# Optimization experiments

Hardware: AMD Instinct MI355X
Metric: run time of the kernel (lower is better)

## Reference

```python
import jax, jax.numpy as jnp
import numpy as np

N = 20000      # bs * n_node
E = 400000     # n_edge
D = 128        # input_nf = hidden_nf
C = 4          # n_channel
ED = 16        # edges_in_d
HS = 4         # mlp_hidden_scale
COORD_MAX = 10.0


def setup_inputs() -> dict:
    key = jax.random.key(0)
    ks = jax.random.split(key, 10)
    h = jax.random.normal(ks[0], (N, D), dtype=jnp.float32)
    coord = jax.random.normal(ks[1], (N, C, 3), dtype=jnp.float32)
    edge_index = jax.random.randint(ks[2], (2, E), 0, N)
    edge_attr = jax.random.normal(ks[3], (E, ED), dtype=jnp.float32)
    kv_in = D + C * C + ED
    Wq = jax.random.normal(ks[4], (D, D), dtype=jnp.float32) * float(1.0 / np.sqrt(D))
    bq = jnp.zeros((D,), dtype=jnp.float32)
    Wkv = jax.random.normal(ks[5], (kv_in, 2 * D), dtype=jnp.float32) * float(1.0 / np.sqrt(kv_in))
    bkv = jnp.zeros((2 * D,), dtype=jnp.float32)
    Wc1 = jax.random.normal(ks[6], (D, HS * D), dtype=jnp.float32) * float(1.0 / np.sqrt(D))
    Wc2 = jax.random.normal(ks[7], (HS * D, C), dtype=jnp.float32) * 0.001  # xavier gain=0.001
    return {"h": h, "coord": coord, "edge_index": edge_index, "edge_attr": edge_attr,
            "Wq": Wq, "bq": bq, "Wkv": Wkv, "bkv": bkv, "Wc1": Wc1, "Wc2": Wc2}


def reference(h, coord, edge_index, edge_attr, Wq, bq, Wkv, bkv, Wc1, Wc2):
    row, col = edge_index[0], edge_index[1]
    n_nodes = h.shape[0]

    # coord2radial (norm_type=None)
    coord_diff = coord[row] - coord[col]                     # [E, C, 3]
    radial = jnp.einsum('ecd,efd->ecf', coord_diff, coord_diff)  # [E, C, C]
    radial = radial.reshape(radial.shape[0], -1)             # [E, C*C]

    # att_model: gather, QKV, scatter-softmax over destination node `row`
    q = h[row] @ Wq + bq                                      # [E, D]
    target_feat = jnp.concatenate([radial, h[col], edge_attr], axis=1)
    kv = target_feat @ Wkv + bkv                               # [E, 2D]
    k, v = kv[:, 0::2], kv[:, 1::2]                            # [E, D] each
    alpha = jnp.sum(q * k, axis=1)                             # [E]
    m = jax.ops.segment_max(alpha, row, num_segments=n_nodes)
    e = jnp.exp(alpha - m[row])
    s = jax.ops.segment_sum(e, row, num_segments=n_nodes)
    att = e / s[row]                                           # [E]

    # node_model (dropout in eval mode = identity)
    agg = jax.ops.segment_sum(att[:, None] * v, row, num_segments=n_nodes)
    h_out = h + agg

    # coord_model: coord_mlp is Linear(no bias) -> SiLU -> Linear(no bias)
    coord_v = att[:, None] * (jax.nn.silu(v @ Wc1) @ Wc2)      # [E, C]
    trans = coord_diff * coord_v[:, :, None]                   # [E, C, 3]
    cagg = jax.ops.segment_sum(trans, row, num_segments=n_nodes)
    coord_out = coord + jnp.clip(cagg, -COORD_MAX, COORD_MAX)

    return (h_out, coord_out, att)
```

## Files before the change

### kernel.cpp

```cpp
#include <hip/hip_runtime.h>

typedef unsigned short u16;
typedef __attribute__((ext_vector_type(8))) short short8;
typedef __attribute__((ext_vector_type(4))) float floatx4;

constexpr int N_ = 20000;
constexpr int E_ = 400000;

#define DEV __device__ __forceinline__

DEV float bf2f(u16 u) { union { unsigned int i; float f; } x; x.i = ((unsigned int)u) << 16; return x.f; }
DEV u16 f2bf(float f) {
    union { unsigned int i; float f; } x; x.f = f;
    unsigned int i = x.i;
    unsigned int r = i + 0x7FFFu + ((i >> 16) & 1u);
    return (u16)(r >> 16);
}
DEV unsigned int fenc(float f) {
    unsigned int i = __float_as_uint(f);
    return (i & 0x80000000u) ? ~i : (i | 0x80000000u);
}
DEV float fdec(unsigned int u) {
    return (u & 0x80000000u) ? __uint_as_float(u ^ 0x80000000u) : __uint_as_float(~u);
}

__global__ __launch_bounds__(256) void k_zero(unsigned int* p, int n) {
    int i = blockIdx.x * 256 + threadIdx.x;
    if (i < n) p[i] = 0u;
}

__global__ __launch_bounds__(256) void k_prep0(
    const float* __restrict__ Wq, const float* __restrict__ bq, const float* __restrict__ Wkv,
    float* __restrict__ M_r, float* __restrict__ M_ea, float* __restrict__ br, float* __restrict__ bea) {
    int o = blockIdx.x * 256 + threadIdx.x;
    if (o < 2048) {
        int k = o >> 4, j = o & 15;
        float acc = 0.f;
        for (int d = 0; d < 128; ++d) acc += Wq[k * 128 + d] * Wkv[(size_t)j * 256 + 2 * d];
        M_r[k * 16 + j] = acc;
    } else if (o < 4096) {
        int k = (o - 2048) >> 4, j = o & 15;
        float acc = 0.f;
        for (int d = 0; d < 128; ++d) acc += Wq[k * 128 + d] * Wkv[(size_t)(144 + j) * 256 + 2 * d];
        M_ea[k * 16 + j] = acc;
    } else if (o < 4112) {
        int j = o - 4096;
        float acc = 0.f;
        for (int d = 0; d < 128; ++d) acc += bq[d] * Wkv[(size_t)j * 256 + 2 * d];
        br[j] = acc;
    } else if (o < 4128) {
        int j = o - 4112;
        float acc = 0.f;
        for (int d = 0; d < 128; ++d) acc += bq[d] * Wkv[(size_t)(144 + j) * 256 + 2 * d];
        bea[j] = acc;
    }
}

__global__ __launch_bounds__(256) void k_prepA(
    const float* __restrict__ Wq, const float* __restrict__ Wkv,
    const float* __restrict__ M_r, const float* __restrict__ M_ea,
    u16* __restrict__ WAf_hi, u16* __restrict__ WAf_lo) {
    int idx = blockIdx.x * 256 + threadIdx.x;
    if (idx >= 6656) return;
    int lane = idx & 63;
    int tkc = idx >> 6;
    int t = tkc >> 2, kc = tkc & 3;
    int col = t * 16 + (lane & 15);
    int k0 = kc * 32 + (lane >> 4) * 8;
#pragma unroll
    for (int j = 0; j < 8; ++j) {
        int k = k0 + j;
        float v;
        if (col < 128)      v = Wq[(size_t)k * 128 + col];
        else if (col < 256) v = Wkv[(size_t)(16 + k) * 256 + 2 * (col - 128)];
        else if (col < 384) v = Wkv[(size_t)(16 + k) * 256 + 2 * (col - 256) + 1];
        else if (col < 400) v = M_r[k * 16 + (col - 384)];
        else                v = M_ea[k * 16 + (col - 400)];
        u16 hi = f2bf(v);
        WAf_hi[(size_t)idx * 8 + j] = hi;
        WAf_lo[(size_t)idx * 8 + j] = f2bf(v - bf2f(hi));
    }
}

__global__ __launch_bounds__(256) void k_prepB(
    const float* __restrict__ Wc1, u16* __restrict__ Wc1f_hi, u16* __restrict__ Wc1f_lo) {
    int idx = blockIdx.x * 256 + threadIdx.x;
    int lane = idx & 63;
    int tkc = idx >> 6;
    int t = tkc >> 2, kc = tkc & 3;
    int jc = t * 16 + (lane & 15);
    int k0 = kc * 32 + (lane >> 4) * 8;
#pragma unroll
    for (int j = 0; j < 8; ++j) {
        float v = Wc1[(size_t)(k0 + j) * 512 + jc];
        u16 hi = f2bf(v);
        Wc1f_hi[(size_t)idx * 8 + j] = hi;
        Wc1f_lo[(size_t)idx * 8 + j] = f2bf(v - bf2f(hi));
    }
}

__global__ __launch_bounds__(256) void k_gemmA(
    const float* __restrict__ h, const u16* __restrict__ WAf_hi, const u16* __restrict__ WAf_lo,
    const float* __restrict__ bq, const float* __restrict__ bkv,
    const float* __restrict__ br, const float* __restrict__ bea,
    float* __restrict__ hq, float* __restrict__ k_h, u16* __restrict__ v_hi16, u16* __restrict__ v_lo16,
    float* __restrict__ hqWkr, float* __restrict__ hqWkea) {
    __shared__ __align__(16) u16 hhi[16][128];
    __shared__ __align__(16) u16 hlo[16][128];
    int t = threadIdx.x;
    int n0 = blockIdx.x * 16;
    for (int i = t; i < 2048; i += 256) {
        int n = i >> 7, d = i & 127;
        float x = h[(size_t)(n0 + n) * 128 + d];
        u16 hi = f2bf(x);
        hhi[n][d] = hi;
        hlo[n][d] = f2bf(x - bf2f(hi));
    }
    __syncthreads();
    int wv = t >> 6, lane = t & 63;
    int m = lane & 15, q = lane >> 4;
    short8 ahi[4], alo[4];
#pragma unroll
    for (int kc = 0; kc < 4; ++kc) {
        ahi[kc] = *(const short8*)(&hhi[m][kc * 32 + q * 8]);
        alo[kc] = *(const short8*)(&hlo[m][kc * 32 + q * 8]);
    }
    for (int tt = wv; tt < 26; tt += 4) {
        floatx4 acc = {0.f, 0.f, 0.f, 0.f};
#pragma unroll
        for (int kc = 0; kc < 4; ++kc) {
            size_t fo = ((size_t)(tt * 4 + kc) * 64 + lane) * 8;
            short8 bhi = *(const short8*)(WAf_hi + fo);
            short8 blo = *(const short8*)(WAf_lo + fo);
            acc = __builtin_amdgcn_mfma_f32_16x16x32_bf16(ahi[kc], bhi, acc, 0, 0, 0);
            acc = __builtin_amdgcn_mfma_f32_16x16x32_bf16(ahi[kc], blo, acc, 0, 0, 0);
            acc = __builtin_amdgcn_mfma_f32_16x16x32_bf16(alo[kc], bhi, acc, 0, 0, 0);
        }
        int col = tt * 16 + m;
        if (tt < 8) {
            float b = bq[col];
#pragma unroll
            for (int reg = 0; reg < 4; ++reg)
                hq[(size_t)(n0 + q * 4 + reg) * 128 + col] = acc[reg] + b;
        } else if (tt < 16) {
            int d = col - 128;
            float b = bkv[2 * d];
#pragma unroll
            for (int reg = 0; reg < 4; ++reg)
                k_h[(size_t)(n0 + q * 4 + reg) * 128 + d] = acc[reg] + b;
        } else if (tt < 24) {
            int d = col - 256;
            float b = bkv[2 * d + 1];
#pragma unroll
            for (int reg = 0; reg < 4; ++reg) {
                float vf = acc[reg] + b;
                u16 hi = f2bf(vf);
                size_t o = (size_t)(n0 + q * 4 + reg) * 128 + d;
                v_hi16[o] = hi;
                v_lo16[o] = f2bf(vf - bf2f(hi));
            }
        } else if (tt == 24) {
            float b = br[m];
#pragma unroll
            for (int reg = 0; reg < 4; ++reg)
                hqWkr[(size_t)(n0 + q * 4 + reg) * 16 + m] = acc[reg] + b;
        } else {
            float b = bea[m];
#pragma unroll
            for (int reg = 0; reg < 4; ++reg)
                hqWkea[(size_t)(n0 + q * 4 + reg) * 16 + m] = acc[reg] + b;
        }
    }
}

__global__ __launch_bounds__(256) void k_gemmB(
    const u16* __restrict__ v_hi16, const u16* __restrict__ v_lo16,
    const u16* __restrict__ Wc1f_hi, const u16* __restrict__ Wc1f_lo,
    u16* __restrict__ vWc1h) {
    int t = threadIdx.x;
    int n0 = blockIdx.x * 16;
    int wv = t >> 6, lane = t & 63;
    int m = lane & 15, q = lane >> 4;
    short8 ahi[4], alo[4];
#pragma unroll
    for (int kc = 0; kc < 4; ++kc) {
        size_t o = (size_t)(n0 + m) * 128 + kc * 32 + q * 8;
        ahi[kc] = *(const short8*)(v_hi16 + o);
        alo[kc] = *(const short8*)(v_lo16 + o);
    }
    for (int tt = wv; tt < 32; tt += 4) {
        floatx4 acc = {0.f, 0.f, 0.f, 0.f};
#pragma unroll
        for (int kc = 0; kc < 4; ++kc) {
            size_t fo = ((size_t)(tt * 4 + kc) * 64 + lane) * 8;
            short8 bhi = *(const short8*)(Wc1f_hi + fo);
            short8 blo = *(const short8*)(Wc1f_lo + fo);
            acc = __builtin_amdgcn_mfma_f32_16x16x32_bf16(ahi[kc], bhi, acc, 0, 0, 0);
            acc = __builtin_amdgcn_mfma_f32_16x16x32_bf16(ahi[kc], blo, acc, 0, 0, 0);
            acc = __builtin_amdgcn_mfma_f32_16x16x32_bf16(alo[kc], bhi, acc, 0, 0, 0);
        }
        int jc = tt * 16 + m;
#pragma unroll
        for (int reg = 0; reg < 4; ++reg)
            vWc1h[(size_t)(n0 + q * 4 + reg) * 512 + jc] = f2bf(acc[reg]);
    }
}

__global__ __launch_bounds__(256) void k_composites(
    const float* __restrict__ Wkv, const float* __restrict__ Wc1,
    float* __restrict__ Cr, float* __restrict__ Cea) {
    int o = blockIdx.x * 256 + threadIdx.x;
    int half = o >> 13;
    int j = (o >> 9) & 15;
    int jc = o & 511;
    int row = half ? (144 + j) : j;
    float acc = 0.f;
    for (int d = 0; d < 128; ++d)
        acc += Wkv[(size_t)row * 256 + 2 * d + 1] * Wc1[(size_t)d * 512 + jc];
    (half ? Cea : Cr)[j * 512 + jc] = acc;
}

__global__ __launch_bounds__(256) void k_hist_both(const int* __restrict__ edge_index,
                                                   int* __restrict__ countsR, int* __restrict__ countsC) {
    int i = blockIdx.x * 256 + threadIdx.x;
    if (i < E_) {
        atomicAdd(&countsR[edge_index[i]], 1);
        atomicAdd(&countsC[edge_index[E_ + i]], 1);
    }
}

__global__ __launch_bounds__(1024) void k_scan2(
    const int* __restrict__ countsR, const int* __restrict__ countsC,
    int* __restrict__ offR, int* __restrict__ curR,
    int* __restrict__ offC, int* __restrict__ curC) {
    __shared__ int wtotR[16], wtotC[16];
    int t = threadIdx.x;
    int lane = t & 63, wv = t >> 6;
    int baseR = 0, baseC = 0;
    for (int start = 0; start < N_; start += 1024) {
        int i = start + t;
        int oR = (i < N_) ? countsR[i] : 0;
        int oC = (i < N_) ? countsC[i] : 0;
        int vR = oR, vC = oC;
#pragma unroll
        for (int off = 1; off < 64; off <<= 1) {
            int xR = __shfl_up(vR, off);
            int xC = __shfl_up(vC, off);
            if (lane >= off) { vR += xR; vC += xC; }
        }
        if (lane == 63) { wtotR[wv] = vR; wtotC[wv] = vC; }
        __syncthreads();
        int wbR = 0, totR = 0, wbC = 0, totC = 0;
#pragma unroll
        for (int k = 0; k < 16; ++k) {
            int wR = wtotR[k], wC = wtotC[k];
            if (k < wv) { wbR += wR; wbC += wC; }
            totR += wR; totC += wC;
        }
        if (i < N_) {
            int eR = baseR + wbR + vR - oR;
            int eC = baseC + wbC + vC - oC;
            offR[i] = eR; curR[i] = eR;
            offC[i] = eC; curC[i] = eC;
        }
        baseR += totR; baseC += totC;
        __syncthreads();
    }
    if (t == 0) { offR[N_] = baseR; offC[N_] = baseC; }
}

__global__ void k_fill_both(const int* __restrict__ edge_index,
                            int* __restrict__ curR, int* __restrict__ curC,
                            int* __restrict__ edge_ids, int* __restrict__ edge_ids2,
                            int* __restrict__ rank2) {
    int i = blockIdx.x * 256 + threadIdx.x;
    if (i < E_) {
        int r = edge_index[i], c = edge_index[E_ + i];
        int pr = atomicAdd(&curR[r], 1);
        edge_ids[pr] = i;
        int pc = atomicAdd(&curC[c], 1);
        edge_ids2[pc] = i;
        rank2[i] = pc;
    }
}

__global__ __launch_bounds__(256) void k_alpha_csr(
    const int* __restrict__ edge_index, const int* __restrict__ edge_ids,
    const float* __restrict__ coord, const float* __restrict__ edge_attr,
    const float* __restrict__ hq, const float* __restrict__ k_h,
    const float* __restrict__ hqWkr, const float* __restrict__ hqWkea,
    float* __restrict__ alpha_pos) {
    int wv = threadIdx.x >> 6, lane = threadIdx.x & 63;
    int p = blockIdx.x * 4 + wv;
    int e = edge_ids[p];
    int row = edge_index[e], col = edge_index[E_ + e];
    float s = hq[(size_t)row * 128 + lane] * k_h[(size_t)col * 128 + lane] +
              hq[(size_t)row * 128 + 64 + lane] * k_h[(size_t)col * 128 + 64 + lane];
    if (lane < 16) {
        int c = lane >> 2, f = lane & 3;
        float rj = 0.f;
#pragma unroll
        for (int x = 0; x < 3; ++x) {
            float a = coord[(size_t)row * 12 + c * 3 + x] - coord[(size_t)col * 12 + c * 3 + x];
            float b = coord[(size_t)row * 12 + f * 3 + x] - coord[(size_t)col * 12 + f * 3 + x];
            rj += a * b;
        }
        s += hqWkr[(size_t)row * 16 + lane] * rj;
    } else if (lane < 32) {
        int j = lane - 16;
        s += hqWkea[(size_t)row * 16 + j] * edge_attr[(size_t)e * 16 + j];
    }
#pragma unroll
    for (int mm = 32; mm; mm >>= 1) s += __shfl_xor(s, mm);
    if (lane == 0) alpha_pos[p] = s;
}

__global__ __launch_bounds__(256, 3) void k_edge_z(
    const int* __restrict__ edge_index, const int* __restrict__ edge_ids2,
    const float* __restrict__ coord, const float* __restrict__ edge_attr,
    const float* __restrict__ Cr, const float* __restrict__ Cea, const float* __restrict__ Wc2,
    const u16* __restrict__ vWc1h, float* __restrict__ Z) {
    __shared__ __align__(16) u16 Bf[32 * 64 * 8];
    __shared__ __align__(16) float W2[512 * 4];
    __shared__ __align__(16) u16 Xs[64][16];
    int t = threadIdx.x;
    for (int i = t; i < 2048; i += 256) {
        int tile = i >> 6, ln = i & 63;
        int jc = tile * 16 + (ln & 15);
        int k0 = (ln >> 4) * 8;
#pragma unroll
        for (int j = 0; j < 8; ++j) {
            int k = k0 + j;
            float v = (k < 16) ? Cr[(size_t)k * 512 + jc] : Cea[(size_t)(k - 16) * 512 + jc];
            Bf[i * 8 + j] = f2bf(v);
        }
    }
    for (int i = t; i < 2048; i += 256) W2[i] = Wc2[i];
    __syncthreads();
    int wv = t >> 6, lane = t & 63;
    int m = lane & 15, q = lane >> 4;
    int wid = blockIdx.x * 4 + wv;
    int nw = gridDim.x * 4;
    for (int ti = wid; ti < E_ / 16; ti += nw) {
        int p0 = ti * 16;
#pragma unroll
        for (int i4 = 0; i4 < 4; ++i4) {
            int e = edge_ids2[p0 + i4 * 4 + q];
            int row = edge_index[e], col = edge_index[E_ + e];
            float d = 0.f;
            if (m < 12) d = coord[(size_t)row * 12 + m] - coord[(size_t)col * 12 + m];
            int base = lane & 48;
            int c3 = (m >> 2) * 3, f3 = (m & 3) * 3;
            float r = 0.f;
#pragma unroll
            for (int x = 0; x < 3; ++x) r += __shfl(d, base + c3 + x) * __shfl(d, base + f3 + x);
            Xs[wv * 16 + i4 * 4 + q][m] = f2bf(r);
        }
        short8 afrag;
        if (q < 2) {
            afrag = *(const short8*)(&Xs[wv * 16 + m][q * 8]);
        } else {
            int em = edge_ids2[p0 + m];
            const float* ea = edge_attr + (size_t)em * 16 + (q - 2) * 8;
#pragma unroll
            for (int j = 0; j < 8; ++j) afrag[j] = (short)f2bf(ea[j]);
        }
        int cr[4];
#pragma unroll
        for (int reg = 0; reg < 4; ++reg) cr[reg] = edge_index[E_ + edge_ids2[p0 + q * 4 + reg]];
        float cvp[4][4];
#pragma unroll
        for (int reg = 0; reg < 4; ++reg)
#pragma unroll
            for (int c = 0; c < 4; ++c) cvp[reg][c] = 0.f;
        for (int tt = 0; tt < 32; ++tt) {
            short8 bfrag = *(const short8*)(Bf + (size_t)(tt * 64 + lane) * 8);
            floatx4 acc = {0.f, 0.f, 0.f, 0.f};
            acc = __builtin_amdgcn_mfma_f32_16x16x32_bf16(afrag, bfrag, acc, 0, 0, 0);
            int jc = tt * 16 + m;
            float4 w2 = *(const float4*)(W2 + jc * 4);
#pragma unroll
            for (int reg = 0; reg < 4; ++reg) {
                float u = acc[reg] + bf2f(vWc1h[(size_t)cr[reg] * 512 + jc]);
                float su = u / (1.f + __expf(-u));
                cvp[reg][0] += su * w2.x;
                cvp[reg][1] += su * w2.y;
                cvp[reg][2] += su * w2.z;
                cvp[reg][3] += su * w2.w;
            }
        }
#pragma unroll
        for (int mm = 1; mm < 16; mm <<= 1)
#pragma unroll
            for (int reg = 0; reg < 4; ++reg)
#pragma unroll
                for (int c = 0; c < 4; ++c) cvp[reg][c] += __shfl_xor(cvp[reg][c], mm);
        if (m < 4) {
#pragma unroll
            for (int reg = 0; reg < 4; ++reg)
                Z[(size_t)(p0 + q * 4 + reg) * 4 + m] = cvp[reg][m];
        }
    }
}

__global__ __launch_bounds__(256) void k_node_main(
    const int* __restrict__ edge_index, const int* __restrict__ offsets, const int* __restrict__ edge_ids,
    const int* __restrict__ rank2, const float* __restrict__ alpha_pos,
    const u16* __restrict__ v_h16, const float* __restrict__ Z,
    const float* __restrict__ coord, const float* __restrict__ edge_attr, const float* __restrict__ h,
    const float* __restrict__ Wkv, float* __restrict__ h_out, float* __restrict__ coord_out,
    float* __restrict__ att_out) {
    __shared__ float attL[4][128];
    int wv = threadIdx.x >> 6, lane = threadIdx.x & 63;
    int n = blockIdx.x * 4 + wv;
    int beg = offsets[n], end = offsets[n + 1];
    float cn[12];
#pragma unroll
    for (int i = 0; i < 12; ++i) cn[i] = coord[(size_t)n * 12 + i];
    float mloc = -3.402823466e38f;
    for (int i = beg + lane; i < end; i += 64) mloc = fmaxf(mloc, alpha_pos[i]);
#pragma unroll
    for (int mm = 32; mm; mm >>= 1) mloc = fmaxf(mloc, __shfl_xor(mloc, mm));
    float sloc = 0.f;
    for (int i = beg + lane; i < end; i += 64) sloc += __expf(alpha_pos[i] - mloc);
#pragma unroll
    for (int mm = 32; mm; mm >>= 1) sloc += __shfl_xor(sloc, mm);
    float inv_s = (end > beg) ? 1.f / sloc : 0.f;
    float raggr[16], eaggr[16], cagg[12];
#pragma unroll
    for (int j = 0; j < 16; ++j) { raggr[j] = 0.f; eaggr[j] = 0.f; }
#pragma unroll
    for (int j = 0; j < 12; ++j) cagg[j] = 0.f;
    for (int ii = lane; ii < end - beg; ii += 64) {
        int i = beg + ii;
        int e = edge_ids[i];
        int col = edge_index[E_ + e];
        float att = __expf(alpha_pos[i] - mloc) * inv_s;
        if (ii < 128) attL[wv][ii] = att;
        att_out[e] = att;
        float cd[12];
#pragma unroll
        for (int x = 0; x < 12; ++x) cd[x] = cn[x] - coord[(size_t)col * 12 + x];
#pragma unroll
        for (int c = 0; c < 4; ++c)
#pragma unroll
            for (int f = 0; f < 4; ++f) {
                float r = cd[c * 3] * cd[f * 3] + cd[c * 3 + 1] * cd[f * 3 + 1] + cd[c * 3 + 2] * cd[f * 3 + 2];
                raggr[c * 4 + f] += att * r;
            }
#pragma unroll
        for (int j = 0; j < 16; ++j) eaggr[j] += att * edge_attr[(size_t)e * 16 + j];
        size_t zb = (size_t)rank2[e] * 4;
        float cv0 = att * Z[zb + 0];
        float cv1 = att * Z[zb + 1];
        float cv2 = att * Z[zb + 2];
        float cv3 = att * Z[zb + 3];
#pragma unroll
        for (int x = 0; x < 3; ++x) {
            cagg[0 + x] += cv0 * cd[0 + x];
            cagg[3 + x] += cv1 * cd[3 + x];
            cagg[6 + x] += cv2 * cd[6 + x];
            cagg[9 + x] += cv3 * cd[9 + x];
        }
    }
#pragma unroll
    for (int mm = 32; mm; mm >>= 1) {
#pragma unroll
        for (int j = 0; j < 16; ++j) {
            raggr[j] += __shfl_xor(raggr[j], mm);
            eaggr[j] += __shfl_xor(eaggr[j], mm);
        }
#pragma unroll
        for (int j = 0; j < 12; ++j) cagg[j] += __shfl_xor(cagg[j], mm);
    }
    float agg0 = 0.f, agg1 = 0.f;
    int deg = end - beg;
    for (int i = 0; i < deg; ++i) {
        int e = edge_ids[beg + i];
        int col = edge_index[E_ + e];
        float att = (i < 128) ? attL[wv][i] : __expf(alpha_pos[beg + i] - mloc) * inv_s;
        agg0 += att * bf2f(v_h16[(size_t)col * 128 + lane]);
        agg1 += att * bf2f(v_h16[(size_t)col * 128 + 64 + lane]);
    }
#pragma unroll
    for (int g = 0; g < 2; ++g) {
        int dd = g * 64 + lane;
        float acc = g ? agg1 : agg0;
#pragma unroll
        for (int j = 0; j < 16; ++j) {
            acc += raggr[j] * Wkv[(size_t)j * 256 + 2 * dd + 1];
            acc += eaggr[j] * Wkv[(size_t)(144 + j) * 256 + 2 * dd + 1];
        }
        h_out[(size_t)n * 128 + dd] = h[(size_t)n * 128 + dd] + acc;
    }
    if (lane == 0) {
#pragma unroll
        for (int i = 0; i < 12; ++i) {
            float v = fminf(fmaxf(cagg[i], -10.f), 10.f);
            coord_out[(size_t)n * 12 + i] = cn[i] + v;
        }
    }
}

__global__ __launch_bounds__(256) void k_hq_slow(
    const float* __restrict__ h, const float* __restrict__ Wq, const float* __restrict__ bq,
    float* __restrict__ hq) {
    int idx = blockIdx.x * 256 + threadIdx.x;
    int n = idx >> 7, d = idx & 127;
    float acc = 0.f;
    for (int k = 0; k < 128; ++k) acc += h[(size_t)n * 128 + k] * Wq[k * 128 + d];
    hq[idx] = acc + bq[d];
}

__global__ __launch_bounds__(256) void k_alpha_slow(
    const int* __restrict__ edge_index, const float* __restrict__ coord,
    const float* __restrict__ edge_attr, const float* __restrict__ h,
    const float* __restrict__ Wkv, const float* __restrict__ bkv,
    const float* __restrict__ hq, float* __restrict__ alpha, unsigned int* __restrict__ m) {
    __shared__ float tf[4][160];
    int wv = threadIdx.x >> 6, lane = threadIdx.x & 63;
    int e = blockIdx.x * 4 + wv;
    int row = edge_index[e], col = edge_index[E_ + e];
    if (lane < 16) {
        int c = lane >> 2, f = lane & 3;
        float rj = 0.f;
#pragma unroll
        for (int x = 0; x < 3; ++x) {
            float a = coord[(size_t)row * 12 + c * 3 + x] - coord[(size_t)col * 12 + c * 3 + x];
            float b = coord[(size_t)row * 12 + f * 3 + x] - coord[(size_t)col * 12 + f * 3 + x];
            rj += a * b;
        }
        tf[wv][lane] = rj;
    }
    for (int f = lane; f < 128; f += 64) tf[wv][16 + f] = h[(size_t)col * 128 + f];
    if (lane >= 48) tf[wv][144 + lane - 48] = edge_attr[(size_t)e * 16 + lane - 48];
    __syncthreads();
    float k0 = bkv[2 * lane], k1 = bkv[2 * (64 + lane)];
    for (int f = 0; f < 160; ++f) {
        float tfv = tf[wv][f];
        k0 += tfv * Wkv[f * 256 + 2 * lane];
        k1 += tfv * Wkv[f * 256 + 128 + 2 * lane];
    }
    float p = hq[(size_t)row * 128 + lane] * k0 + hq[(size_t)row * 128 + 64 + lane] * k1;
#pragma unroll
    for (int mm = 32; mm; mm >>= 1) p += __shfl_xor(p, mm);
    if (lane == 0) {
        alpha[e] = p;
        atomicMax(&m[row], fenc(p));
    }
}

__global__ __launch_bounds__(256) void k_expsum_slow(
    const int* __restrict__ edge_index, const float* __restrict__ alpha,
    const unsigned int* __restrict__ m, float* __restrict__ s) {
    int e = blockIdx.x * 256 + threadIdx.x;
    if (e < E_) {
        int row = edge_index[e];
        atomicAdd(&s[row], __expf(alpha[e] - fdec(m[row])));
    }
}

__global__ __launch_bounds__(256) void k_edge2_slow(
    const int* __restrict__ edge_index, const float* __restrict__ coord,
    const float* __restrict__ edge_attr, const float* __restrict__ h,
    const float* __restrict__ Wkv, const float* __restrict__ bkv,
    const float* __restrict__ Wc1, const float* __restrict__ Wc2,
    const float* __restrict__ alpha, const unsigned int* __restrict__ m, const float* __restrict__ s,
    float* __restrict__ agg, float* __restrict__ cagg, float* __restrict__ att_out) {
    __shared__ float tf[4][160];
    __shared__ float vsh[4][128];
    int wv = threadIdx.x >> 6, lane = threadIdx.x & 63;
    int e = blockIdx.x * 4 + wv;
    int row = edge_index[e], col = edge_index[E_ + e];
    if (lane < 16) {
        int c = lane >> 2, f = lane & 3;
        float rj = 0.f;
#pragma unroll
        for (int x = 0; x < 3; ++x) {
            float a = coord[(size_t)row * 12 + c * 3 + x] - coord[(size_t)col * 12 + c * 3 + x];
            float b = coord[(size_t)row * 12 + f * 3 + x] - coord[(size_t)col * 12 + f * 3 + x];
            rj += a * b;
        }
        tf[wv][lane] = rj;
    }
    for (int f = lane; f < 128; f += 64) tf[wv][16 + f] = h[(size_t)col * 128 + f];
    if (lane >= 48) tf[wv][144 + lane - 48] = edge_attr[(size_t)e * 16 + lane - 48];
    __syncthreads();
    float v0 = bkv[2 * lane + 1], v1 = bkv[2 * (64 + lane) + 1];
    for (int f = 0; f < 160; ++f) {
        float tfv = tf[wv][f];
        v0 += tfv * Wkv[f * 256 + 2 * lane + 1];
        v1 += tfv * Wkv[f * 256 + 129 + 2 * lane];
    }
    float att = __expf(alpha[e] - fdec(m[row])) / s[row];
    atomicAdd(&agg[(size_t)row * 128 + lane], att * v0);
    atomicAdd(&agg[(size_t)row * 128 + 64 + lane], att * v1);
    vsh[wv][lane] = v0;
    vsh[wv][64 + lane] = v1;
    __syncthreads();
    float cv[4] = {0.f, 0.f, 0.f, 0.f};
    for (int g = 0; g < 8; ++g) {
        int jc = g * 64 + lane;
        float u = 0.f;
        for (int dd = 0; dd < 128; ++dd) u += vsh[wv][dd] * Wc1[dd * 512 + jc];
        float su = u / (1.f + __expf(-u));
#pragma unroll
        for (int c = 0; c < 4; ++c) cv[c] += su * Wc2[jc * 4 + c];
    }
#pragma unroll
    for (int mm = 32; mm; mm >>= 1)
#pragma unroll
        for (int c = 0; c < 4; ++c) cv[c] += __shfl_xor(cv[c], mm);
    if (lane < 12) {
        int c = lane / 3;
        float cd = coord[(size_t)row * 12 + lane] - coord[(size_t)col * 12 + lane];
        atomicAdd(&cagg[(size_t)row * 12 + lane], att * cv[c] * cd);
    }
    if (lane == 0) att_out[e] = att;
}

__global__ __launch_bounds__(256) void k_final_slow(
    const float* __restrict__ h, const float* __restrict__ coord,
    const float* __restrict__ agg, const float* __restrict__ cagg,
    float* __restrict__ h_out, float* __restrict__ coord_out) {
    int idx = blockIdx.x * 256 + threadIdx.x;
    h_out[idx] = h[idx] + agg[idx];
    if (idx < N_ * 12) {
        float v = fminf(fmaxf(cagg[idx], -10.f), 10.f);
        coord_out[idx] = coord[idx] + v;
    }
}

extern "C" void kernel_launch(void* const* d_in, const int* in_sizes, int n_in,
                              void* d_out, int out_size, void* d_ws, size_t ws_size,
                              hipStream_t stream) {
    (void)in_sizes; (void)n_in; (void)out_size;
    const float* h          = (const float*)d_in[0];
    const float* coord      = (const float*)d_in[1];
    const int*   edge_index = (const int*)d_in[2];
    const float* edge_attr  = (const float*)d_in[3];
    const float* Wq         = (const float*)d_in[4];
    const float* bq         = (const float*)d_in[5];
    const float* Wkv        = (const float*)d_in[6];
    const float* bkv        = (const float*)d_in[7];
    const float* Wc1        = (const float*)d_in[8];
    const float* Wc2        = (const float*)d_in[9];

    float* out = (float*)d_out;
    float* h_out = out;
    float* coord_out = out + (size_t)N_ * 128;
    float* att_out = coord_out + (size_t)N_ * 12;

    char* w = (char*)d_ws;
    size_t off = 0;
    auto alloc = [&](size_t bytes) -> void* {
        void* p = w + off;
        off += (bytes + 255) & ~(size_t)255;
        return p;
    };
    int* countsR   = (int*)alloc((size_t)2 * N_ * 4);
    int* countsC   = countsR + N_;
    float* hq      = (float*)alloc((size_t)N_ * 128 * 4);
    float* k_h     = (float*)alloc((size_t)N_ * 128 * 4);
    u16*   v_h16   = (u16*)alloc((size_t)N_ * 128 * 2);
    u16*   v_lo16  = (u16*)alloc((size_t)N_ * 128 * 2);
    u16*   vWc1h   = (u16*)alloc((size_t)N_ * 512 * 2);
    float* hqWkr   = (float*)alloc((size_t)N_ * 16 * 4);
    float* hqWkea  = (float*)alloc((size_t)N_ * 16 * 4);
    float* alphaP  = (float*)alloc((size_t)E_ * 4);
    float* Z       = (float*)alloc((size_t)E_ * 4 * 4);
    float* Cr      = (float*)alloc(16 * 512 * 4);
    float* Cea     = (float*)alloc(16 * 512 * 4);
    float* M_r     = (float*)alloc(128 * 16 * 4);
    float* M_ea    = (float*)alloc(128 * 16 * 4);
    float* br      = (float*)alloc(16 * 4);
    float* bea     = (float*)alloc(16 * 4);
    u16* WAf_hi    = (u16*)alloc((size_t)26 * 4 * 64 * 8 * 2);
    u16* WAf_lo    = (u16*)alloc((size_t)26 * 4 * 64 * 8 * 2);
    u16* Wc1f_hi   = (u16*)alloc((size_t)32 * 4 * 64 * 8 * 2);
    u16* Wc1f_lo   = (u16*)alloc((size_t)32 * 4 * 64 * 8 * 2);
    int* offsetsR  = (int*)alloc((size_t)(N_ + 1) * 4);
    int* cursorR   = (int*)alloc((size_t)N_ * 4);
    int* edge_ids  = (int*)alloc((size_t)E_ * 4);
    int* offsetsC  = (int*)alloc((size_t)(N_ + 1) * 4);
    int* cursorC   = (int*)alloc((size_t)N_ * 4);
    int* edge_ids2 = (int*)alloc((size_t)E_ * 4);
    int* rank2     = (int*)alloc((size_t)E_ * 4);
    size_t fast_req = off;

    if (ws_size >= fast_req) {
        hipLaunchKernelGGL(k_zero, dim3((2 * N_ + 255) / 256), dim3(256), 0, stream,
                           (unsigned int*)countsR, 2 * N_);
        hipLaunchKernelGGL(k_hist_both, dim3((E_ + 255) / 256), dim3(256), 0, stream,
                           edge_index, countsR, countsC);
        hipLaunchKernelGGL(k_scan2, dim3(1), dim3(1024), 0, stream,
                           countsR, countsC, offsetsR, cursorR, offsetsC, cursorC);
        hipLaunchKernelGGL(k_fill_both, dim3((E_ + 255) / 256), dim3(256), 0, stream,
                           edge_index, cursorR, cursorC, edge_ids, edge_ids2, rank2);
        hipLaunchKernelGGL(k_prep0, dim3(17), dim3(256), 0, stream,
                           Wq, bq, Wkv, M_r, M_ea, br, bea);
        hipLaunchKernelGGL(k_prepA, dim3(26), dim3(256), 0, stream,
                           Wq, Wkv, M_r, M_ea, WAf_hi, WAf_lo);
        hipLaunchKernelGGL(k_prepB, dim3(32), dim3(256), 0, stream,
                           Wc1, Wc1f_hi, Wc1f_lo);
        hipLaunchKernelGGL(k_composites, dim3(64), dim3(256), 0, stream, Wkv, Wc1, Cr, Cea);
        hipLaunchKernelGGL(k_gemmA, dim3(N_ / 16), dim3(256), 0, stream,
                           h, WAf_hi, WAf_lo, bq, bkv, br, bea,
                           hq, k_h, v_h16, v_lo16, hqWkr, hqWkea);
        hipLaunchKernelGGL(k_gemmB, dim3(N_ / 16), dim3(256), 0, stream,
                           v_h16, v_lo16, Wc1f_hi, Wc1f_lo, vWc1h);
        hipLaunchKernelGGL(k_alpha_csr, dim3(E_ / 4), dim3(256), 0, stream,
                           edge_index, edge_ids, coord, edge_attr, hq, k_h, hqWkr, hqWkea, alphaP);
        hipLaunchKernelGGL(k_edge_z, dim3(768), dim3(256), 0, stream,
                           edge_index, edge_ids2, coord, edge_attr, Cr, Cea, Wc2, vWc1h, Z);
        hipLaunchKernelGGL(k_node_main, dim3(N_ / 4), dim3(256), 0, stream,
                           edge_index, offsetsR, edge_ids, rank2, alphaP, v_h16, Z,
                           coord, edge_attr, h, Wkv, h_out, coord_out, att_out);
    } else {
        off = 0;
        float* s        = (float*)alloc((size_t)N_ * 4);
        unsigned int* m = (unsigned int*)alloc((size_t)N_ * 4);
        float* agg      = (float*)alloc((size_t)N_ * 128 * 4);
        float* cagg     = (float*)alloc((size_t)N_ * 12 * 4);
        size_t zb       = off;
        float* hq2      = (float*)alloc((size_t)N_ * 128 * 4);
        float* alpha2   = (float*)alloc((size_t)E_ * 4);
        int zero_n = (int)(zb / 4);
        hipLaunchKernelGGL(k_zero, dim3((zero_n + 255) / 256), dim3(256), 0, stream,
                           (unsigned int*)s, zero_n);
        hipLaunchKernelGGL(k_hq_slow, dim3(N_ * 128 / 256), dim3(256), 0, stream, h, Wq, bq, hq2);
        hipLaunchKernelGGL(k_alpha_slow, dim3(E_ / 4), dim3(256), 0, stream,
                           edge_index, coord, edge_attr, h, Wkv, bkv, hq2, alpha2, m);
        hipLaunchKernelGGL(k_expsum_slow, dim3((E_ + 255) / 256), dim3(256), 0, stream,
                           edge_index, alpha2, m, s);
        hipLaunchKernelGGL(k_edge2_slow, dim3(E_ / 4), dim3(256), 0, stream,
                           edge_index, coord, edge_attr, h, Wkv, bkv, Wc1, Wc2,
                           alpha2, m, s, agg, cagg, att_out);
        hipLaunchKernelGGL(k_final_slow, dim3(N_ * 128 / 256), dim3(256), 0, stream,
                           h, coord, agg, cagg, h_out, coord_out);
    }
}
```

Measured before the change: 810.6 us.

## Swizzle vWc1 layout for vector loads and index Z by edge id

```diff
diff --git a/kernel.cpp b/kernel.cpp
--- a/kernel.cpp
+++ b/kernel.cpp
@@ -176,7 +176,7 @@
 __global__ __launch_bounds__(256) void k_gemmB(
     const u16* __restrict__ v_hi16, const u16* __restrict__ v_lo16,
     const u16* __restrict__ Wc1f_hi, const u16* __restrict__ Wc1f_lo,
-    u16* __restrict__ vWc1h) {
+    u16* __restrict__ vWc1s) {
     int t = threadIdx.x;
     int n0 = blockIdx.x * 16;
     int wv = t >> 6, lane = t & 63;
@@ -199,10 +199,9 @@
             acc = __builtin_amdgcn_mfma_f32_16x16x32_bf16(ahi[kc], blo, acc, 0, 0, 0);
             acc = __builtin_amdgcn_mfma_f32_16x16x32_bf16(alo[kc], bhi, acc, 0, 0, 0);
         }
-        int jc = tt * 16 + m;
 #pragma unroll
         for (int reg = 0; reg < 4; ++reg)
-            vWc1h[(size_t)(n0 + q * 4 + reg) * 512 + jc] = f2bf(acc[reg]);
+            vWc1s[(size_t)(n0 + q * 4 + reg) * 512 + m * 32 + tt] = f2bf(acc[reg]);
     }
 }
 
@@ -271,8 +270,7 @@
 
 __global__ void k_fill_both(const int* __restrict__ edge_index,
                             int* __restrict__ curR, int* __restrict__ curC,
-                            int* __restrict__ edge_ids, int* __restrict__ edge_ids2,
-                            int* __restrict__ rank2) {
+                            int* __restrict__ edge_ids, int* __restrict__ edge_ids2) {
     int i = blockIdx.x * 256 + threadIdx.x;
     if (i < E_) {
         int r = edge_index[i], c = edge_index[E_ + i];
@@ -280,7 +278,6 @@
         edge_ids[pr] = i;
         int pc = atomicAdd(&curC[c], 1);
         edge_ids2[pc] = i;
-        rank2[i] = pc;
     }
 }
 
@@ -319,7 +316,7 @@
     const int* __restrict__ edge_index, const int* __restrict__ edge_ids2,
     const float* __restrict__ coord, const float* __restrict__ edge_attr,
     const float* __restrict__ Cr, const float* __restrict__ Cea, const float* __restrict__ Wc2,
-    const u16* __restrict__ vWc1h, float* __restrict__ Z) {
+    const u16* __restrict__ vWc1s, float* __restrict__ Z) {
     __shared__ __align__(16) u16 Bf[32 * 64 * 8];
     __shared__ __align__(16) float W2[512 * 4];
     __shared__ __align__(16) u16 Xs[64][16];
@@ -365,28 +362,39 @@
 #pragma unroll
             for (int j = 0; j < 8; ++j) afrag[j] = (short)f2bf(ea[j]);
         }
-        int cr[4];
-#pragma unroll
-        for (int reg = 0; reg < 4; ++reg) cr[reg] = edge_index[E_ + edge_ids2[p0 + q * 4 + reg]];
+        int er[4], cr[4];
+#pragma unroll
+        for (int reg = 0; reg < 4; ++reg) {
+            er[reg] = edge_ids2[p0 + q * 4 + reg];
+            cr[reg] = edge_index[E_ + er[reg]];
+        }
         float cvp[4][4];
 #pragma unroll
         for (int reg = 0; reg < 4; ++reg)
 #pragma unroll
             for (int c = 0; c < 4; ++c) cvp[reg][c] = 0.f;
-        for (int tt = 0; tt < 32; ++tt) {
-            short8 bfrag = *(const short8*)(Bf + (size_t)(tt * 64 + lane) * 8);
-            floatx4 acc = {0.f, 0.f, 0.f, 0.f};
-            acc = __builtin_amdgcn_mfma_f32_16x16x32_bf16(afrag, bfrag, acc, 0, 0, 0);
-            int jc = tt * 16 + m;
-            float4 w2 = *(const float4*)(W2 + jc * 4);
-#pragma unroll
-            for (int reg = 0; reg < 4; ++reg) {
-                float u = acc[reg] + bf2f(vWc1h[(size_t)cr[reg] * 512 + jc]);
-                float su = u / (1.f + __expf(-u));
-                cvp[reg][0] += su * w2.x;
-                cvp[reg][1] += su * w2.y;
-                cvp[reg][2] += su * w2.z;
-                cvp[reg][3] += su * w2.w;
+        for (int cc = 0; cc < 4; ++cc) {
+            short8 vv[4];
+#pragma unroll
+            for (int reg = 0; reg < 4; ++reg)
+                vv[reg] = *(const short8*)(vWc1s + (size_t)cr[reg] * 512 + m * 32 + cc * 8);
+#pragma unroll
+            for (int tj = 0; tj < 8; ++tj) {
+                int tt = cc * 8 + tj;
+                short8 bfrag = *(const short8*)(Bf + (size_t)(tt * 64 + lane) * 8);
+                floatx4 acc = {0.f, 0.f, 0.f, 0.f};
+                acc = __builtin_amdgcn_mfma_f32_16x16x32_bf16(afrag, bfrag, acc, 0, 0, 0);
+                int jc = tt * 16 + m;
+                float4 w2 = *(const float4*)(W2 + jc * 4);
+#pragma unroll
+                for (int reg = 0; reg < 4; ++reg) {
+                    float u = acc[reg] + bf2f((u16)vv[reg][tj]);
+                    float su = u / (1.f + __expf(-u));
+                    cvp[reg][0] += su * w2.x;
+                    cvp[reg][1] += su * w2.y;
+                    cvp[reg][2] += su * w2.z;
+                    cvp[reg][3] += su * w2.w;
+                }
             }
         }
 #pragma unroll
@@ -398,14 +406,14 @@
         if (m < 4) {
 #pragma unroll
             for (int reg = 0; reg < 4; ++reg)
-                Z[(size_t)(p0 + q * 4 + reg) * 4 + m] = cvp[reg][m];
+                Z[(size_t)er[reg] * 4 + m] = cvp[reg][m];
         }
     }
 }
 
 __global__ __launch_bounds__(256) void k_node_main(
     const int* __restrict__ edge_index, const int* __restrict__ offsets, const int* __restrict__ edge_ids,
-    const int* __restrict__ rank2, const float* __restrict__ alpha_pos,
+    const float* __restrict__ alpha_pos,
     const u16* __restrict__ v_h16, const float* __restrict__ Z,
     const float* __restrict__ coord, const float* __restrict__ edge_attr, const float* __restrict__ h,
     const float* __restrict__ Wkv, float* __restrict__ h_out, float* __restrict__ coord_out,
@@ -450,7 +458,7 @@
             }
 #pragma unroll
         for (int j = 0; j < 16; ++j) eaggr[j] += att * edge_attr[(size_t)e * 16 + j];
-        size_t zb = (size_t)rank2[e] * 4;
+        size_t zb = (size_t)e * 4;
         float cv0 = att * Z[zb + 0];
         float cv1 = att * Z[zb + 1];
         float cv2 = att * Z[zb + 2];
@@ -664,7 +672,7 @@
     float* k_h     = (float*)alloc((size_t)N_ * 128 * 4);
     u16*   v_h16   = (u16*)alloc((size_t)N_ * 128 * 2);
     u16*   v_lo16  = (u16*)alloc((size_t)N_ * 128 * 2);
-    u16*   vWc1h   = (u16*)alloc((size_t)N_ * 512 * 2);
+    u16*   vWc1s   = (u16*)alloc((size_t)N_ * 512 * 2);
     float* hqWkr   = (float*)alloc((size_t)N_ * 16 * 4);
     float* hqWkea  = (float*)alloc((size_t)N_ * 16 * 4);
     float* alphaP  = (float*)alloc((size_t)E_ * 4);
@@ -685,7 +693,6 @@
     int* offsetsC  = (int*)alloc((size_t)(N_ + 1) * 4);
     int* cursorC   = (int*)alloc((size_t)N_ * 4);
     int* edge_ids2 = (int*)alloc((size_t)E_ * 4);
-    int* rank2     = (int*)alloc((size_t)E_ * 4);
     size_t fast_req = off;
 
     if (ws_size >= fast_req) {
@@ -696,7 +703,7 @@
         hipLaunchKernelGGL(k_scan2, dim3(1), dim3(1024), 0, stream,
                            countsR, countsC, offsetsR, cursorR, offsetsC, cursorC);
         hipLaunchKernelGGL(k_fill_both, dim3((E_ + 255) / 256), dim3(256), 0, stream,
-                           edge_index, cursorR, cursorC, edge_ids, edge_ids2, rank2);
+                           edge_index, cursorR, cursorC, edge_ids, edge_ids2);
         hipLaunchKernelGGL(k_prep0, dim3(17), dim3(256), 0, stream,
                            Wq, bq, Wkv, M_r, M_ea, br, bea);
         hipLaunchKernelGGL(k_prepA, dim3(26), dim3(256), 0, stream,
@@ -708,13 +715,13 @@
                            h, WAf_hi, WAf_lo, bq, bkv, br, bea,
                            hq, k_h, v_h16, v_lo16, hqWkr, hqWkea);
         hipLaunchKernelGGL(k_gemmB, dim3(N_ / 16), dim3(256), 0, stream,
-                           v_h16, v_lo16, Wc1f_hi, Wc1f_lo, vWc1h);
+                           v_h16, v_lo16, Wc1f_hi, Wc1f_lo, vWc1s);
         hipLaunchKernelGGL(k_alpha_csr, dim3(E_ / 4), dim3(256), 0, stream,
                            edge_index, edge_ids, coord, edge_attr, hq, k_h, hqWkr, hqWkea, alphaP);
         hipLaunchKernelGGL(k_edge_z, dim3(768), dim3(256), 0, stream,
-                           edge_index, edge_ids2, coord, edge_attr, Cr, Cea, Wc2, vWc1h, Z);
+                           edge_index, edge_ids2, coord, edge_attr, Cr, Cea, Wc2, vWc1s, Z);
         hipLaunchKernelGGL(k_node_main, dim3(N_ / 4), dim3(256), 0, stream,
-                           edge_index, offsetsR, edge_ids, rank2, alphaP, v_h16, Z,
+                           edge_index, offsetsR, edge_ids, alphaP, v_h16, Z,
                            coord, edge_attr, h, Wkv, h_out, coord_out, att_out);
     } else {
         off = 0;
```

Result: no change. 823.3 us (+1.6%).
